# Performance work log

Hardware: AMD Instinct MI355X
Metric: run time of the kernel (lower is better)

Reference implementation:

```python
import jax, jax.numpy as jnp
import numpy as np


def setup_inputs() -> dict:
    key = jax.random.key(0)
    ks = jax.random.split(key, 6)
    B, N, D, E = 16, 64, 256, 256
    nodes = jax.random.normal(ks[0], (B * N, D), jnp.float32)
    edges = jax.random.normal(ks[1], (B * N * N, E), jnp.float32)
    W_in = jax.random.normal(ks[2], (2 * D + E, D), jnp.float32) / np.float32(np.sqrt(2 * D + E))
    b_in = jnp.zeros((D,), jnp.float32)
    W_coef = jax.random.normal(ks[3], (D, 1), jnp.float32) / np.float32(np.sqrt(D))
    b_coef = jnp.zeros((1,), jnp.float32)
    W_out = jax.random.normal(ks[4], (D, D), jnp.float32) / np.float32(np.sqrt(D))
    b_out = jnp.zeros((D,), jnp.float32)
    return {"nodes": nodes, "edges": edges, "W_in": W_in, "b_in": b_in,
            "W_coef": W_coef, "b_coef": b_coef, "W_out": W_out, "b_out": b_out,
            "B": B, "N": N}


def reference(nodes, edges, W_in, b_in, W_coef, b_coef, W_out, b_out, B, N):
    # Uniform nums = [N]*B special case of the ragged torch loop.
    D = nodes.shape[-1]
    n3 = nodes.reshape(B, N, D)
    # pair[b,i,j] = [node_i, node_j, edge_ij]  -> [B,N,N,2D+E]
    pair = jnp.concatenate([
        jnp.broadcast_to(n3[:, :, None, :], (B, N, N, D)),
        jnp.broadcast_to(n3[:, None, :, :], (B, N, N, D)),
        edges.reshape(B, N, N, -1),
    ], axis=-1)
    h = jax.nn.relu(pair @ W_in + b_in)            # [B,N,N,D]
    coefs = h @ W_coef + b_coef                    # [B,N,N,1]
    diag = jnp.eye(N, dtype=coefs.dtype)[None, :, :, None] * jnp.float32(1e9)
    attn = jax.nn.softmax(coefs - diag, axis=2)    # softmax over j, diag masked
    residual = jnp.sum(attn * h, axis=2)           # [B,N,D]
    new_nodes = nodes + jax.nn.relu(residual.reshape(B * N, D) @ W_out + b_out)
    return new_nodes, h.reshape(B * N * N, D)
```

## Files before the change

### kernel.cpp

```cpp
#include <hip/hip_runtime.h>
#include <hip/hip_bf16.h>

typedef unsigned int u32;
typedef unsigned short u16;
typedef __attribute__((ext_vector_type(8))) short bf16x8;
typedef __attribute__((ext_vector_type(4))) float f32x4;

#define DI __device__ __forceinline__

DI u16 f2bfu(float f){
  union{float f; u32 i;} u; u.f = f;
  u32 lsb = (u.i >> 16) & 1u;
  u.i += 0x7fffu + lsb;
  return (u16)(u.i >> 16);
}

union BU { uint4 v; bf16x8 s; };

__global__ __launch_bounds__(256) void k_pack(const float* __restrict__ W_in,
                                              u16* __restrict__ Wp3,
                                              u16* __restrict__ Wp12)
{
  int idx = blockIdx.x * 256 + threadIdx.x;
  int l = idx & 63;
  int g = idx >> 6;
  int lq = l >> 4, lr = l & 15;
  u16 o[8];
  if (g < 128){
    int nt = g >> 3, kk = g & 7;
    int n  = nt * 16 + lr;
    int k0 = 512 + kk * 32 + lq * 8;
#pragma unroll
    for (int tt = 0; tt < 8; tt++) o[tt] = f2bfu(W_in[(size_t)(k0 + tt) * 256 + n]);
    *(uint4*)(Wp3 + (size_t)idx * 8) = *(uint4*)o;
  } else {
    int g2 = g - 128;
    int half = g2 >> 7, rem = g2 & 127;
    int nt = rem >> 3, kk = rem & 7;
    int n  = nt * 16 + lr;
    int k0 = half * 256 + kk * 32 + lq * 8;
#pragma unroll
    for (int tt = 0; tt < 8; tt++) o[tt] = f2bfu(W_in[(size_t)(k0 + tt) * 256 + n]);
    *(uint4*)(Wp12 + (size_t)g2 * 512 + (size_t)l * 8) = *(uint4*)o;
  }
}

__global__ __launch_bounds__(256) void k_pre(
    const float* __restrict__ nodes, const float* __restrict__ b_in,
    const u16* __restrict__ Wp12, float* __restrict__ P1, float* __restrict__ P2)
{
  const int t = threadIdx.x;
  const int w = t >> 6, l = t & 63, lq = l >> 4, lr = l & 15;
  const int rt = blockIdx.x >> 1, half = blockIdx.x & 1;

  bf16x8 af[8];
  {
    const float* ap = nodes + (size_t)(rt * 64 + 16 * w + lr) * 256 + lq * 8;
#pragma unroll
    for (int kk = 0; kk < 8; kk++){
      float4 x = *(const float4*)(ap + kk * 32);
      float4 y = *(const float4*)(ap + kk * 32 + 4);
      bf16x8 a;
      a[0]=(short)f2bfu(x.x); a[1]=(short)f2bfu(x.y); a[2]=(short)f2bfu(x.z); a[3]=(short)f2bfu(x.w);
      a[4]=(short)f2bfu(y.x); a[5]=(short)f2bfu(y.y); a[6]=(short)f2bfu(y.z); a[7]=(short)f2bfu(y.w);
      af[kk] = a;
    }
  }
  const uint4* wp = (const uint4*)(Wp12 + (size_t)half * 128 * 512);
  float* P = half ? P2 : P1;
#pragma unroll
  for (int nt = 0; nt < 16; nt++){
    f32x4 acc = {0.f, 0.f, 0.f, 0.f};
#pragma unroll
    for (int kk = 0; kk < 8; kk++){
      BU bu; bu.v = wp[(nt * 8 + kk) * 64 + l];
      acc = __builtin_amdgcn_mfma_f32_16x16x32_bf16(af[kk], bu.s, acc, 0, 0, 0);
    }
    const int col = nt * 16 + lr;
    const float bv = half ? 0.f : b_in[col];
#pragma unroll
    for (int r = 0; r < 4; r++){
      const int row = rt * 64 + 16 * w + 4 * lq + r;
      P[(size_t)row * 256 + col] = acc[r] + bv;
    }
  }
}

__global__ __launch_bounds__(256) void k_main(
    const float* __restrict__ nodes, const float* __restrict__ edges,
    const u16* __restrict__ Wp3, const float* __restrict__ W_coef,
    const float* __restrict__ b_coef, const float* __restrict__ W_out,
    const float* __restrict__ b_out, const float* __restrict__ P1,
    const float* __restrict__ P2, float* __restrict__ out_nodes,
    float* __restrict__ out_h)
{
  __shared__ float hS[64 * 256];
  __shared__ float coefS[64];
  __shared__ float attnS[64];
  __shared__ float resS[256];

  const int t = threadIdx.x;
  const int w = t >> 6, l = t & 63, lq = l >> 4, lr = l & 15;
  const int bi = blockIdx.x;
  const int b = bi >> 6, i = bi & 63;

  bf16x8 af[8];
  {
    const float* ap = edges + (size_t)bi * 16384 + (size_t)(16 * w + lr) * 256 + lq * 8;
#pragma unroll
    for (int kk = 0; kk < 8; kk++){
      float4 x = *(const float4*)(ap + kk * 32);
      float4 y = *(const float4*)(ap + kk * 32 + 4);
      bf16x8 a;
      a[0]=(short)f2bfu(x.x); a[1]=(short)f2bfu(x.y); a[2]=(short)f2bfu(x.z); a[3]=(short)f2bfu(x.w);
      a[4]=(short)f2bfu(y.x); a[5]=(short)f2bfu(y.y); a[6]=(short)f2bfu(y.z); a[7]=(short)f2bfu(y.w);
      af[kk] = a;
    }
  }

  const uint4* wp = (const uint4*)Wp3;
  float cpart[4] = {0.f, 0.f, 0.f, 0.f};
#pragma unroll
  for (int nt = 0; nt < 16; nt++){
    f32x4 acc = {0.f, 0.f, 0.f, 0.f};
#pragma unroll
    for (int kk = 0; kk < 8; kk++){
      BU bu; bu.v = wp[(nt * 8 + kk) * 64 + l];
      acc = __builtin_amdgcn_mfma_f32_16x16x32_bf16(af[kk], bu.s, acc, 0, 0, 0);
    }
    const int col = nt * 16 + lr;
    const float p1 = P1[(size_t)bi * 256 + col];
    const float wc = W_coef[col];
#pragma unroll
    for (int r = 0; r < 4; r++){
      const int row = 16 * w + 4 * lq + r;
      const float p2 = P2[((size_t)b * 64 + row) * 256 + col];
      float h = acc[r] + p1 + p2;
      h = h > 0.f ? h : 0.f;
      hS[row * 256 + col] = h;
      out_h[((size_t)bi * 64 + row) * 256 + col] = h;
      cpart[r] += h * wc;
    }
  }

#pragma unroll
  for (int r = 0; r < 4; r++){
    float v = cpart[r];
    v += __shfl_xor(v, 1, 64);
    v += __shfl_xor(v, 2, 64);
    v += __shfl_xor(v, 4, 64);
    v += __shfl_xor(v, 8, 64);
    if (lr == 0) coefS[16 * w + 4 * lq + r] = v;
  }
  __syncthreads();

  if (t < 64){
    int j = t;
    float val = coefS[j] + b_coef[0] - (j == i ? 1e9f : 0.f);
    float m = val;
#pragma unroll
    for (int off = 32; off >= 1; off >>= 1){ float o = __shfl_xor(m, off, 64); m = m > o ? m : o; }
    float e = __expf(val - m);
    float s = e;
#pragma unroll
    for (int off = 32; off >= 1; off >>= 1) s += __shfl_xor(s, off, 64);
    attnS[j] = e / s;
  }
  __syncthreads();

  {
    const int d = t;
    float res = 0.f;
#pragma unroll 8
    for (int j = 0; j < 64; j++) res += attnS[j] * hS[j * 256 + d];
    resS[d] = res;
  }
  __syncthreads();

  {
    const int d = t;
    float acco = b_out[d];
    for (int k4 = 0; k4 < 64; k4++){
      float4 r4 = *(const float4*)&resS[k4 * 4];
      acco += r4.x * W_out[(size_t)(k4 * 4 + 0) * 256 + d];
      acco += r4.y * W_out[(size_t)(k4 * 4 + 1) * 256 + d];
      acco += r4.z * W_out[(size_t)(k4 * 4 + 2) * 256 + d];
      acco += r4.w * W_out[(size_t)(k4 * 4 + 3) * 256 + d];
    }
    float nv = nodes[(size_t)bi * 256 + d];
    out_nodes[(size_t)bi * 256 + d] = nv + (acco > 0.f ? acco : 0.f);
  }
}

extern "C" void kernel_launch(void* const* d_in, const int* in_sizes, int n_in,
                              void* d_out, int out_size, void* d_ws, size_t ws_size,
                              hipStream_t stream)
{
  const float* nodes  = (const float*)d_in[0];
  const float* edges  = (const float*)d_in[1];
  const float* W_in   = (const float*)d_in[2];
  const float* b_in   = (const float*)d_in[3];
  const float* W_coef = (const float*)d_in[4];
  const float* b_coef = (const float*)d_in[5];
  const float* W_out  = (const float*)d_in[6];
  const float* b_out  = (const float*)d_in[7];
  (void)in_sizes; (void)n_in; (void)out_size; (void)ws_size;

  float* P1  = (float*)d_ws;
  float* P2  = P1 + 262144;
  u16*  Wp3  = (u16*)(P2 + 262144);
  u16*  Wp12 = Wp3 + 65536;

  float* out_nodes = (float*)d_out;
  float* out_h = out_nodes + 262144;

  hipLaunchKernelGGL(k_pack, dim3(96),   dim3(256), 0, stream, W_in, Wp3, Wp12);
  hipLaunchKernelGGL(k_pre,  dim3(32),   dim3(256), 0, stream, nodes, b_in, Wp12, P1, P2);
  hipLaunchKernelGGL(k_main, dim3(1024), dim3(256), 0, stream,
                     nodes, edges, Wp3, W_coef, b_coef, W_out, b_out,
                     P1, P2, out_nodes, out_h);
}
```

Baseline: 183.8 us.

## Store h tile as bf16 in LDS, coalesce h output, widen pre-GEMM grid

The main kernel now keeps the h tile in LDS as padded bf16 instead of fp32, which halves shared memory and allows four blocks per CU via launch bounds. The h output is written afterwards from LDS with coalesced vector stores rather than scattered per-element stores. The P2 loads are hoisted ahead of the MFMA loop. The node-projection kernel reads and converts W_in directly across a grid eight times wider, which removes the packing of those weights. Rounding h to bf16 before writing the h output and computing the attention sum adds precision error to both.

```diff
diff --git a/kernel.cpp b/kernel.cpp
--- a/kernel.cpp
+++ b/kernel.cpp
@@ -8,50 +8,38 @@
 
 #define DI __device__ __forceinline__
 
-DI u16 f2bfu(float f){
-  union{float f; u32 i;} u; u.f = f;
-  u32 lsb = (u.i >> 16) & 1u;
-  u.i += 0x7fffu + lsb;
-  return (u16)(u.i >> 16);
-}
+DI u16 f2b(float f){
+  __hip_bfloat16 b = __float2bfloat16(f);
+  union{__hip_bfloat16 b; u16 u;} c; c.b = b; return c.u;
+}
+DI float b2f(u16 u){ union{u32 i; float f;} c; c.i = ((u32)u) << 16; return c.f; }
 
 union BU { uint4 v; bf16x8 s; };
 
+#define HS_STRIDE 264
+
 __global__ __launch_bounds__(256) void k_pack(const float* __restrict__ W_in,
-                                              u16* __restrict__ Wp3,
-                                              u16* __restrict__ Wp12)
+                                              u16* __restrict__ Wp3)
 {
   int idx = blockIdx.x * 256 + threadIdx.x;
-  int l = idx & 63;
-  int g = idx >> 6;
+  int l = idx & 63, g = idx >> 6;
+  int nt = g >> 3, kk = g & 7;
   int lq = l >> 4, lr = l & 15;
+  int n  = nt * 16 + lr;
+  int k0 = 512 + kk * 32 + lq * 8;
   u16 o[8];
-  if (g < 128){
-    int nt = g >> 3, kk = g & 7;
-    int n  = nt * 16 + lr;
-    int k0 = 512 + kk * 32 + lq * 8;
-#pragma unroll
-    for (int tt = 0; tt < 8; tt++) o[tt] = f2bfu(W_in[(size_t)(k0 + tt) * 256 + n]);
-    *(uint4*)(Wp3 + (size_t)idx * 8) = *(uint4*)o;
-  } else {
-    int g2 = g - 128;
-    int half = g2 >> 7, rem = g2 & 127;
-    int nt = rem >> 3, kk = rem & 7;
-    int n  = nt * 16 + lr;
-    int k0 = half * 256 + kk * 32 + lq * 8;
-#pragma unroll
-    for (int tt = 0; tt < 8; tt++) o[tt] = f2bfu(W_in[(size_t)(k0 + tt) * 256 + n]);
-    *(uint4*)(Wp12 + (size_t)g2 * 512 + (size_t)l * 8) = *(uint4*)o;
-  }
+#pragma unroll
+  for (int tt = 0; tt < 8; tt++) o[tt] = f2b(W_in[(size_t)(k0 + tt) * 256 + n]);
+  *(uint4*)(Wp3 + (size_t)idx * 8) = *(uint4*)o;
 }
 
 __global__ __launch_bounds__(256) void k_pre(
     const float* __restrict__ nodes, const float* __restrict__ b_in,
-    const u16* __restrict__ Wp12, float* __restrict__ P1, float* __restrict__ P2)
+    const float* __restrict__ W_in, float* __restrict__ P1, float* __restrict__ P2)
 {
   const int t = threadIdx.x;
   const int w = t >> 6, l = t & 63, lq = l >> 4, lr = l & 15;
-  const int rt = blockIdx.x >> 1, half = blockIdx.x & 1;
+  const int rt = blockIdx.x >> 4, half = (blockIdx.x >> 3) & 1, ntp = blockIdx.x & 7;
 
   bf16x8 af[8];
   {
@@ -61,32 +49,36 @@
       float4 x = *(const float4*)(ap + kk * 32);
       float4 y = *(const float4*)(ap + kk * 32 + 4);
       bf16x8 a;
-      a[0]=(short)f2bfu(x.x); a[1]=(short)f2bfu(x.y); a[2]=(short)f2bfu(x.z); a[3]=(short)f2bfu(x.w);
-      a[4]=(short)f2bfu(y.x); a[5]=(short)f2bfu(y.y); a[6]=(short)f2bfu(y.z); a[7]=(short)f2bfu(y.w);
+      a[0]=(short)f2b(x.x); a[1]=(short)f2b(x.y); a[2]=(short)f2b(x.z); a[3]=(short)f2b(x.w);
+      a[4]=(short)f2b(y.x); a[5]=(short)f2b(y.y); a[6]=(short)f2b(y.z); a[7]=(short)f2b(y.w);
       af[kk] = a;
     }
   }
-  const uint4* wp = (const uint4*)(Wp12 + (size_t)half * 128 * 512);
   float* P = half ? P2 : P1;
 #pragma unroll
-  for (int nt = 0; nt < 16; nt++){
+  for (int q = 0; q < 2; q++){
+    const int nt = ntp * 2 + q;
+    const int n  = nt * 16 + lr;
     f32x4 acc = {0.f, 0.f, 0.f, 0.f};
 #pragma unroll
     for (int kk = 0; kk < 8; kk++){
-      BU bu; bu.v = wp[(nt * 8 + kk) * 64 + l];
+      const int k0 = half * 256 + kk * 32 + lq * 8;
+      u16 o[8];
+#pragma unroll
+      for (int tt = 0; tt < 8; tt++) o[tt] = f2b(W_in[(size_t)(k0 + tt) * 256 + n]);
+      BU bu; bu.v = *(uint4*)o;
       acc = __builtin_amdgcn_mfma_f32_16x16x32_bf16(af[kk], bu.s, acc, 0, 0, 0);
     }
-    const int col = nt * 16 + lr;
-    const float bv = half ? 0.f : b_in[col];
+    const float bv = half ? 0.f : b_in[n];
 #pragma unroll
     for (int r = 0; r < 4; r++){
       const int row = rt * 64 + 16 * w + 4 * lq + r;
-      P[(size_t)row * 256 + col] = acc[r] + bv;
-    }
-  }
-}
-
-__global__ __launch_bounds__(256) void k_main(
+      P[(size_t)row * 256 + n] = acc[r] + bv;
+    }
+  }
+}
+
+__global__ __launch_bounds__(256, 4) void k_main(
     const float* __restrict__ nodes, const float* __restrict__ edges,
     const u16* __restrict__ Wp3, const float* __restrict__ W_coef,
     const float* __restrict__ b_coef, const float* __restrict__ W_out,
@@ -94,7 +86,7 @@
     const float* __restrict__ P2, float* __restrict__ out_nodes,
     float* __restrict__ out_h)
 {
-  __shared__ float hS[64 * 256];
+  __shared__ u16 hS[64 * HS_STRIDE];
   __shared__ float coefS[64];
   __shared__ float attnS[64];
   __shared__ float resS[256];
@@ -112,8 +104,8 @@
       float4 x = *(const float4*)(ap + kk * 32);
       float4 y = *(const float4*)(ap + kk * 32 + 4);
       bf16x8 a;
-      a[0]=(short)f2bfu(x.x); a[1]=(short)f2bfu(x.y); a[2]=(short)f2bfu(x.z); a[3]=(short)f2bfu(x.w);
-      a[4]=(short)f2bfu(y.x); a[5]=(short)f2bfu(y.y); a[6]=(short)f2bfu(y.z); a[7]=(short)f2bfu(y.w);
+      a[0]=(short)f2b(x.x); a[1]=(short)f2b(x.y); a[2]=(short)f2b(x.z); a[3]=(short)f2b(x.w);
+      a[4]=(short)f2b(y.x); a[5]=(short)f2b(y.y); a[6]=(short)f2b(y.z); a[7]=(short)f2b(y.w);
       af[kk] = a;
     }
   }
@@ -122,23 +114,26 @@
   float cpart[4] = {0.f, 0.f, 0.f, 0.f};
 #pragma unroll
   for (int nt = 0; nt < 16; nt++){
-    f32x4 acc = {0.f, 0.f, 0.f, 0.f};
-#pragma unroll
-    for (int kk = 0; kk < 8; kk++){
-      BU bu; bu.v = wp[(nt * 8 + kk) * 64 + l];
-      acc = __builtin_amdgcn_mfma_f32_16x16x32_bf16(af[kk], bu.s, acc, 0, 0, 0);
-    }
     const int col = nt * 16 + lr;
     const float p1 = P1[(size_t)bi * 256 + col];
     const float wc = W_coef[col];
+    float p2v[4];
+#pragma unroll
+    for (int r = 0; r < 4; r++)
+      p2v[r] = P2[((size_t)b * 64 + 16 * w + 4 * lq + r) * 256 + col];
+
+    f32x4 acc = {0.f, 0.f, 0.f, 0.f};
+#pragma unroll
+    for (int kk = 0; kk < 8; kk++){
+      BU bu; bu.v = wp[(nt * 8 + kk) * 64 + l];
+      acc = __builtin_amdgcn_mfma_f32_16x16x32_bf16(af[kk], bu.s, acc, 0, 0, 0);
+    }
 #pragma unroll
     for (int r = 0; r < 4; r++){
       const int row = 16 * w + 4 * lq + r;
-      const float p2 = P2[((size_t)b * 64 + row) * 256 + col];
-      float h = acc[r] + p1 + p2;
+      float h = acc[r] + p1 + p2v[r];
       h = h > 0.f ? h : 0.f;
-      hS[row * 256 + col] = h;
-      out_h[((size_t)bi * 64 + row) * 256 + col] = h;
+      hS[row * HS_STRIDE + col] = f2b(h);
       cpart[r] += h * wc;
     }
   }
@@ -166,13 +161,27 @@
     for (int off = 32; off >= 1; off >>= 1) s += __shfl_xor(s, off, 64);
     attnS[j] = e / s;
   }
+
+  {
+    float* op = out_h + (size_t)bi * 16384;
+#pragma unroll
+    for (int q = 0; q < 8; q++){
+      int idx = q * 256 + t;
+      int row = idx >> 5, c8 = (idx & 31) * 8;
+      uint4 v = *(const uint4*)(hS + row * HS_STRIDE + c8);
+      const u16* e = (const u16*)&v;
+      float* dp = op + row * 256 + c8;
+      *(float4*)dp       = make_float4(b2f(e[0]), b2f(e[1]), b2f(e[2]), b2f(e[3]));
+      *(float4*)(dp + 4) = make_float4(b2f(e[4]), b2f(e[5]), b2f(e[6]), b2f(e[7]));
+    }
+  }
   __syncthreads();
 
   {
     const int d = t;
     float res = 0.f;
 #pragma unroll 8
-    for (int j = 0; j < 64; j++) res += attnS[j] * hS[j * 256 + d];
+    for (int j = 0; j < 64; j++) res += attnS[j] * b2f(hS[j * HS_STRIDE + d]);
     resS[d] = res;
   }
   __syncthreads();
@@ -209,13 +218,12 @@
   float* P1  = (float*)d_ws;
   float* P2  = P1 + 262144;
   u16*  Wp3  = (u16*)(P2 + 262144);
-  u16*  Wp12 = Wp3 + 65536;
 
   float* out_nodes = (float*)d_out;
   float* out_h = out_nodes + 262144;
 
-  hipLaunchKernelGGL(k_pack, dim3(96),   dim3(256), 0, stream, W_in, Wp3, Wp12);
-  hipLaunchKernelGGL(k_pre,  dim3(32),   dim3(256), 0, stream, nodes, b_in, Wp12, P1, P2);
+  hipLaunchKernelGGL(k_pack, dim3(32),   dim3(256), 0, stream, W_in, Wp3);
+  hipLaunchKernelGGL(k_pre,  dim3(256),  dim3(256), 0, stream, nodes, b_in, W_in, P1, P2);
   hipLaunchKernelGGL(k_main, dim3(1024), dim3(256), 0, stream,
                      nodes, edges, Wp3, W_coef, b_coef, W_out, b_out,
                      P1, P2, out_nodes, out_h);
```

Result: slower. 190.3 us (+3.6%).
